# Kernel optimization log

Hardware: AMD Instinct MI355X
Metric: run time of the kernel (lower is better)

Reference implementation:

```python
import jax, jax.numpy as jnp
import numpy as np

N_NODES = 100000
N_EDGES = 1600000
D_IN = 128
D_HID = 128
D_OUT = 16


def gcn_conv(x, W, b, src, dst, deg_inv_sqrt, deg_inv):
    # PyG GCNConv: transform then normalized aggregate with self-loops.
    h = x @ W  # [N, H]
    norm = deg_inv_sqrt[src] * deg_inv_sqrt[dst]  # [E]
    msg = h[src] * norm[:, None]  # [E, H] gather
    agg = jax.ops.segment_sum(msg, dst, num_segments=N_NODES)  # scatter-add
    agg = agg + h * deg_inv[:, None]  # self-loop term (weight deg^-1)
    return agg + b


def setup_inputs() -> dict:
    key = jax.random.key(0)
    ks = jax.random.split(key, 10)
    x = jax.random.normal(ks[0], (N_NODES, D_IN), dtype=jnp.float32)
    edge_index = jax.random.randint(ks[1], (2, N_EDGES), 0, N_NODES)
    s = 1.0 / np.sqrt(D_IN)
    sh = 1.0 / np.sqrt(D_HID)
    W0 = jax.random.uniform(ks[2], (D_IN, D_HID), jnp.float32, -s, s)
    b0 = jnp.zeros((D_HID,), jnp.float32)
    W1 = jax.random.uniform(ks[3], (D_HID, D_HID), jnp.float32, -sh, sh)
    b1 = jnp.zeros((D_HID,), jnp.float32)
    W2 = jax.random.uniform(ks[4], (D_HID, D_HID), jnp.float32, -sh, sh)
    b2 = jnp.zeros((D_HID,), jnp.float32)
    Wr = jax.random.uniform(ks[5], (D_HID, D_OUT), jnp.float32, -sh, sh)
    br = jax.random.uniform(ks[6], (D_OUT,), jnp.float32, -sh, sh)
    return {"x": x, "edge_index": edge_index, "W0": W0, "b0": b0,
            "W1": W1, "b1": b1, "W2": W2, "b2": b2, "Wr": Wr, "br": br}


def reference(x, edge_index, W0, b0, W1, b1, W2, b2, Wr, br):
    src, dst = edge_index[0], edge_index[1]
    # degree with self-loops: deg[i] = 1 + indegree(i)
    deg = jax.ops.segment_sum(jnp.ones((N_EDGES,), x.dtype), dst,
                              num_segments=N_NODES) + 1.0
    deg_inv_sqrt = deg ** -0.5
    deg_inv = 1.0 / deg
    h = x
    for W, b in ((W0, b0), (W1, b1), (W2, b2)):
        h = gcn_conv(h, W, b, src, dst, deg_inv_sqrt, deg_inv)
        h = jax.nn.relu(h)  # dropout is identity at inference
    out = h @ Wr + br
    return jax.nn.sigmoid(out) * 0.8 + 0.1
```

## Files before the change

kernel.cpp:

```cpp
#include <hip/hip_runtime.h>
#include <math.h>

#define N_NODES 100000
#define N_EDGES 1600000
#define NBUCKET 782
#define EB      256
#define EPB     6250


static __device__ __forceinline__ unsigned short f2bf(float f) {
    unsigned int u = __float_as_uint(f);
    unsigned int r = (u + 0x7FFFu + ((u >> 16) & 1u)) >> 16;
    return (unsigned short)r;
}
static __device__ __forceinline__ float bf2f(unsigned short h) {
    return __uint_as_float(((unsigned int)h) << 16);
}


__global__ __launch_bounds__(256) void hist_kernel(const int* __restrict__ dst,
                                                   int* __restrict__ hist ) {
    __shared__ int h[NBUCKET];
    int tid = threadIdx.x;
    for (int b = tid; b < NBUCKET; b += 256) h[b] = 0;
    __syncthreads();
    int base = blockIdx.x * EPB;
    for (int i = tid; i < EPB; i += 256)
        atomicAdd(&h[dst[base + i] >> 7], 1);
    __syncthreads();
    int* hrow = hist + (size_t)blockIdx.x * NBUCKET;
    for (int b = tid; b < NBUCKET; b += 256) hrow[b] = h[b];
}

__global__ __launch_bounds__(256) void scan_hist_kernel(const int* __restrict__ hist,
                                                        int* __restrict__ blkoffT,
                                                        int* __restrict__ btotal) {
    __shared__ int s[256];
    int b = blockIdx.x;
    int k = threadIdx.x;
    int v = hist[(size_t)k * NBUCKET + b];
    s[k] = v;
    __syncthreads();
    for (int off = 1; off < 256; off <<= 1) {
        int t = 0;
        if (k >= off) t = s[k - off];
        __syncthreads();
        s[k] += t;
        __syncthreads();
    }
    blkoffT[(size_t)b * 256 + k] = s[k] - v;
    if (k == 255) btotal[b] = s[255];
}

__global__ __launch_bounds__(256) void bucket_scan_kernel(const int* __restrict__ btotal,
                                                          int* __restrict__ bucket_start) {
    __shared__ int cs[256];
    int tid = threadIdx.x;
    int base = tid * 4;
    int v[4];
    int sum = 0;
#pragma unroll
    for (int q = 0; q < 4; q++) {
        int idx = base + q;
        v[q] = (idx < NBUCKET) ? btotal[idx] : 0;
        sum += v[q];
    }
    cs[tid] = sum;
    __syncthreads();
    for (int off = 1; off < 256; off <<= 1) {
        int t = 0;
        if (tid >= off) t = cs[tid - off];
        __syncthreads();
        cs[tid] += t;
        __syncthreads();
    }
    int run = cs[tid] - sum;
#pragma unroll
    for (int q = 0; q < 4; q++) {
        int idx = base + q;
        if (idx < NBUCKET + 1) bucket_start[idx] = run;
        run += v[q];
    }
}

__global__ __launch_bounds__(256) void scatter_kernel(const int* __restrict__ src,
                                                      const int* __restrict__ dst,
                                                      const int* __restrict__ blkoffT,
                                                      const int* __restrict__ bucket_start,
                                                      int* __restrict__ pairs) {
    __shared__ int cur[NBUCKET];
    int tid = threadIdx.x;
    for (int b = tid; b < NBUCKET; b += 256)
        cur[b] = bucket_start[b] + blkoffT[(size_t)b * 256 + blockIdx.x];
    __syncthreads();
    int base = blockIdx.x * EPB;
    for (int i = tid; i < EPB; i += 256) {
        int d = dst[base + i];
        int s = src[base + i];
        int pos = atomicAdd(&cur[d >> 7], 1);
        pairs[pos] = s | ((d & 127) << 20);
    }
}

__global__ __launch_bounds__(256) void build_csr_kernel(const int* __restrict__ pairs,
                                                        const int* __restrict__ bucket_start,
                                                        int* __restrict__ rowstart,
                                                        int* __restrict__ counts,
                                                        float* __restrict__ dis,
                                                        int* __restrict__ csr_src) {
    __shared__ int lcnt[128];
    __shared__ int lsc[128];
    __shared__ int lcur[128];
    int tid = threadIdx.x;
    int b = blockIdx.x;
    int node_base = b * 128;
    if (tid < 128) lcnt[tid] = 0;
    __syncthreads();
    int rs = bucket_start[b];
    int re = bucket_start[b + 1];
    for (int e = rs + tid; e < re; e += 256)
        atomicAdd(&lcnt[pairs[e] >> 20], 1);
    __syncthreads();
    if (tid < 128) lsc[tid] = lcnt[tid];
    __syncthreads();
    for (int off = 1; off < 128; off <<= 1) {
        int t = 0;
        if (tid < 128 && tid >= off) t = lsc[tid - off];
        __syncthreads();
        if (tid < 128) lsc[tid] += t;
        __syncthreads();
    }
    if (tid < 128) {
        int node = node_base + tid;
        if (node < N_NODES) {
            int startg = rs + lsc[tid] - lcnt[tid];
            rowstart[node] = startg;
            counts[node]   = lcnt[tid];
            dis[node]      = rsqrtf((float)(lcnt[tid] + 1));
            lcur[tid]      = startg;
        }
    }
    __syncthreads();
    for (int e = rs + tid; e < re; e += 256) {
        int v = pairs[e];
        int pos = atomicAdd(&lcur[v >> 20], 1);
        csr_src[pos] = v & 0xFFFFF;
    }
}


__global__ __launch_bounds__(256) void gemm128_kernel(const float* __restrict__ X,
                                                      const float* __restrict__ W,
                                                      const float* __restrict__ scale,
                                                      unsigned short* __restrict__ Yb,
                                                      int nrows) {
    __shared__ float As[16][132];
    __shared__ float Bs[16][128];
    int tid = threadIdx.x;
    int tx = tid & 15;
    int ty = tid >> 4;
    int rowBase = blockIdx.x * 128;

    float acc[8][8];
#pragma unroll
    for (int i = 0; i < 8; i++)
#pragma unroll
        for (int j = 0; j < 8; j++) acc[i][j] = 0.f;

    int a_r  = tid >> 1;
    int a_k4 = (tid & 1) * 8;

    for (int kb = 0; kb < 128; kb += 16) {
        {
            int grow = rowBase + a_r;
            float4 v0 = make_float4(0.f,0.f,0.f,0.f), v1 = v0;
            if (grow < nrows) {
                v0 = *(const float4*)&X[(size_t)grow * 128 + kb + a_k4];
                v1 = *(const float4*)&X[(size_t)grow * 128 + kb + a_k4 + 4];
            }
            As[a_k4 + 0][a_r] = v0.x; As[a_k4 + 1][a_r] = v0.y;
            As[a_k4 + 2][a_r] = v0.z; As[a_k4 + 3][a_r] = v0.w;
            As[a_k4 + 4][a_r] = v1.x; As[a_k4 + 5][a_r] = v1.y;
            As[a_k4 + 6][a_r] = v1.z; As[a_k4 + 7][a_r] = v1.w;
        }
        {
            int f0 = tid, f1 = tid + 256;
            *(float4*)&Bs[f0 >> 5][(f0 & 31) * 4] =
                *(const float4*)&W[(size_t)(kb + (f0 >> 5)) * 128 + (f0 & 31) * 4];
            *(float4*)&Bs[f1 >> 5][(f1 & 31) * 4] =
                *(const float4*)&W[(size_t)(kb + (f1 >> 5)) * 128 + (f1 & 31) * 4];
        }
        __syncthreads();
#pragma unroll
        for (int kk = 0; kk < 16; kk++) {
            float4 a0 = *(const float4*)&As[kk][ty * 8];
            float4 a1 = *(const float4*)&As[kk][ty * 8 + 4];
            float4 b0 = *(const float4*)&Bs[kk][tx * 8];
            float4 b1 = *(const float4*)&Bs[kk][tx * 8 + 4];
            float a[8] = {a0.x,a0.y,a0.z,a0.w,a1.x,a1.y,a1.z,a1.w};
            float b[8] = {b0.x,b0.y,b0.z,b0.w,b1.x,b1.y,b1.z,b1.w};
#pragma unroll
            for (int i = 0; i < 8; i++)
#pragma unroll
                for (int j = 0; j < 8; j++) acc[i][j] = fmaf(a[i], b[j], acc[i][j]);
        }
        __syncthreads();
    }
#pragma unroll
    for (int i = 0; i < 8; i++) {
        int grow = rowBase + ty * 8 + i;
        if (grow < nrows) {
            float s = scale[grow];
            unsigned int p0 = (unsigned int)f2bf(acc[i][0]*s) | ((unsigned int)f2bf(acc[i][1]*s) << 16);
            unsigned int p1 = (unsigned int)f2bf(acc[i][2]*s) | ((unsigned int)f2bf(acc[i][3]*s) << 16);
            unsigned int p2 = (unsigned int)f2bf(acc[i][4]*s) | ((unsigned int)f2bf(acc[i][5]*s) << 16);
            unsigned int p3 = (unsigned int)f2bf(acc[i][6]*s) | ((unsigned int)f2bf(acc[i][7]*s) << 16);
            uint4 pk = make_uint4(p0, p1, p2, p3);
            *(uint4*)&Yb[(size_t)grow * 128 + tx * 8] = pk;
        }
    }
}


__global__ __launch_bounds__(256) void aggregate_kernel(const unsigned short* __restrict__ Hs,
                                                        const float* __restrict__ dis,
                                                        const int* __restrict__ rowstart,
                                                        const int* __restrict__ counts,
                                                        const int* __restrict__ csr_src,
                                                        const float* __restrict__ bias,
                                                        float* __restrict__ Out) {
    int node = blockIdx.x * 4 + (threadIdx.x >> 6);
    node = __builtin_amdgcn_readfirstlane(node);
    int lane = threadIdx.x & 63;
    if (node >= N_NODES) return;
    int c0 = lane * 2;

    unsigned int ow = *(const unsigned int*)&Hs[(size_t)node * 128 + c0];
    float accx = bf2f((unsigned short)(ow & 0xffffu));
    float accy = bf2f((unsigned short)(ow >> 16));

    int start = rowstart[node];
    int cnt   = counts[node];
    int end = start + cnt;
    int j = start;

    for (; j + 7 < end; j += 8) {
        int s0 = __builtin_nontemporal_load(&csr_src[j]);
        int s1 = __builtin_nontemporal_load(&csr_src[j + 1]);
        int s2 = __builtin_nontemporal_load(&csr_src[j + 2]);
        int s3 = __builtin_nontemporal_load(&csr_src[j + 3]);
        int s4 = __builtin_nontemporal_load(&csr_src[j + 4]);
        int s5 = __builtin_nontemporal_load(&csr_src[j + 5]);
        int s6 = __builtin_nontemporal_load(&csr_src[j + 6]);
        int s7 = __builtin_nontemporal_load(&csr_src[j + 7]);
        unsigned int w0 = *(const unsigned int*)&Hs[(size_t)s0 * 128 + c0];
        unsigned int w1 = *(const unsigned int*)&Hs[(size_t)s1 * 128 + c0];
        unsigned int w2 = *(const unsigned int*)&Hs[(size_t)s2 * 128 + c0];
        unsigned int w3 = *(const unsigned int*)&Hs[(size_t)s3 * 128 + c0];
        unsigned int w4 = *(const unsigned int*)&Hs[(size_t)s4 * 128 + c0];
        unsigned int w5 = *(const unsigned int*)&Hs[(size_t)s5 * 128 + c0];
        unsigned int w6 = *(const unsigned int*)&Hs[(size_t)s6 * 128 + c0];
        unsigned int w7 = *(const unsigned int*)&Hs[(size_t)s7 * 128 + c0];
        accx += ((bf2f((unsigned short)(w0 & 0xffffu)) + bf2f((unsigned short)(w1 & 0xffffu)))
               + (bf2f((unsigned short)(w2 & 0xffffu)) + bf2f((unsigned short)(w3 & 0xffffu))))
              + ((bf2f((unsigned short)(w4 & 0xffffu)) + bf2f((unsigned short)(w5 & 0xffffu)))
               + (bf2f((unsigned short)(w6 & 0xffffu)) + bf2f((unsigned short)(w7 & 0xffffu))));
        accy += ((bf2f((unsigned short)(w0 >> 16)) + bf2f((unsigned short)(w1 >> 16)))
               + (bf2f((unsigned short)(w2 >> 16)) + bf2f((unsigned short)(w3 >> 16))))
              + ((bf2f((unsigned short)(w4 >> 16)) + bf2f((unsigned short)(w5 >> 16)))
               + (bf2f((unsigned short)(w6 >> 16)) + bf2f((unsigned short)(w7 >> 16))));
    }
    for (; j + 1 < end; j += 2) {
        int s0 = __builtin_nontemporal_load(&csr_src[j]);
        int s1 = __builtin_nontemporal_load(&csr_src[j + 1]);
        unsigned int w0 = *(const unsigned int*)&Hs[(size_t)s0 * 128 + c0];
        unsigned int w1 = *(const unsigned int*)&Hs[(size_t)s1 * 128 + c0];
        accx += bf2f((unsigned short)(w0 & 0xffffu)) + bf2f((unsigned short)(w1 & 0xffffu));
        accy += bf2f((unsigned short)(w0 >> 16)) + bf2f((unsigned short)(w1 >> 16));
    }
    if (j < end) {
        int s0 = __builtin_nontemporal_load(&csr_src[j]);
        unsigned int w0 = *(const unsigned int*)&Hs[(size_t)s0 * 128 + c0];
        accx += bf2f((unsigned short)(w0 & 0xffffu));
        accy += bf2f((unsigned short)(w0 >> 16));
    }

    float dsi = dis[node];
    float2 bb = *(const float2*)&bias[c0];
    float2 r;
    r.x = fmaxf(fmaf(accx, dsi, bb.x), 0.f);
    r.y = fmaxf(fmaf(accy, dsi, bb.y), 0.f);
    unsigned long long bits;
    __builtin_memcpy(&bits, &r, 8);
    __builtin_nontemporal_store(bits, (unsigned long long*)&Out[(size_t)node * 128 + c0]);
}


__global__ __launch_bounds__(256) void final_kernel(const float* __restrict__ H,
                                                    const float* __restrict__ Wr,
                                                    const float* __restrict__ br,
                                                    float* __restrict__ out) {
    __shared__ float hs[16][132];
    __shared__ float ws[128][16];
    int tid = threadIdx.x;
    int rowBase = blockIdx.x * 16;
    {
        int k  = tid & 127;
        int r0 = tid >> 7;
#pragma unroll
        for (int rr = 0; rr < 8; rr++) {
            int r = r0 + rr * 2;
            int grow = rowBase + r;
            hs[r][k] = (grow < N_NODES) ? H[(size_t)grow * 128 + k] : 0.f;
        }
#pragma unroll
        for (int q = 0; q < 8; q++) {
            int idx = q * 256 + tid;
            ws[idx >> 4][idx & 15] = Wr[idx];
        }
    }
    __syncthreads();
    int row = tid >> 4;
    int c   = tid & 15;
    float acc = br[c];
#pragma unroll
    for (int k = 0; k < 128; k++)
        acc = fmaf(hs[row][k], ws[k][c], acc);
    int grow = rowBase + row;
    if (grow < N_NODES) {
        float sg = 1.f / (1.f + expf(-acc));
        out[(size_t)grow * 16 + c] = 0.8f * sg + 0.1f;
    }
}


extern "C" void kernel_launch(void* const* d_in, const int* in_sizes, int n_in,
                              void* d_out, int out_size, void* d_ws, size_t ws_size,
                              hipStream_t stream) {
    const float* x  = (const float*)d_in[0];
    const int*   ei = (const int*)d_in[1];
    const int*   src = ei;
    const int*   dst = ei + N_EDGES;
    const float* W0 = (const float*)d_in[2];
    const float* b0 = (const float*)d_in[3];
    const float* W1 = (const float*)d_in[4];
    const float* b1 = (const float*)d_in[5];
    const float* W2 = (const float*)d_in[6];
    const float* b2 = (const float*)d_in[7];
    const float* Wr = (const float*)d_in[8];
    const float* br = (const float*)d_in[9];
    float* out = (float*)d_out;

    char* ws = (char*)d_ws;
    size_t off = 0;
    auto take = [&](size_t bytes) {
        char* p = ws + off;
        off += (bytes + 255) & ~(size_t)255;
        return p;
    };
    float*          hA       = (float*)take((size_t)N_NODES * 128 * 4);
    unsigned short* hBs      = (unsigned short*)take((size_t)N_NODES * 128 * 2);
    int*            counts   = (int*)take((size_t)N_NODES * 4);
    int*            rowstart = (int*)take((size_t)N_NODES * 4);
    float*          dis      = (float*)take((size_t)N_NODES * 4);
    int*            csr_src  = (int*)take((size_t)N_EDGES * 4);
    int*            pairs    = (int*)take((size_t)N_EDGES * 4);
    int*            hist     = (int*)take((size_t)EB * NBUCKET * 4);
    int*            blkoffT  = (int*)take((size_t)NBUCKET * EB * 4);
    int*            btotal   = (int*)take(1024 * 4);
    int*            bstart   = (int*)take(1024 * 4);
    (void)ws_size; (void)in_sizes; (void)n_in; (void)out_size;

    hist_kernel<<<EB, 256, 0, stream>>>(dst, hist);
    scan_hist_kernel<<<NBUCKET, 256, 0, stream>>>(hist, blkoffT, btotal);
    bucket_scan_kernel<<<1, 256, 0, stream>>>(btotal, bstart);
    scatter_kernel<<<EB, 256, 0, stream>>>(src, dst, blkoffT, bstart, pairs);
    build_csr_kernel<<<NBUCKET, 256, 0, stream>>>(pairs, bstart, rowstart, counts, dis, csr_src);

    const float* Wl[3] = {W0, W1, W2};
    const float* bl[3] = {b0, b1, b2};
    const float* hin = x;
    for (int l = 0; l < 3; l++) {
        gemm128_kernel<<<(N_NODES + 127) / 128, 256, 0, stream>>>(hin, Wl[l], dis, hBs, N_NODES);
        aggregate_kernel<<<N_NODES / 4, 256, 0, stream>>>(hBs, dis, rowstart, counts,
                                                          csr_src, bl[l], hA);
        hin = hA;
    }
    final_kernel<<<N_NODES / 16, 256, 0, stream>>>(hA, Wr, br, out);
}
```

Baseline: 543.7 us.

## Use bf16 MFMA GEMM and store hidden activations as bf16

Replaces the fp32 FMA tiled GEMM with a bf16 MFMA kernel (16x16x32) that uses swizzled LDS tiles. It adds conversion kernels for x and a transposed W. The aggregate kernel now writes bf16 activations instead of fp32, so the next GEMM and the final kernel read half the bytes. The cost is lower precision in the GEMM inputs and intermediate activations, plus extra conversion launches and scalar 2-byte stores in the GEMM epilogue.

```diff
diff --git a/kernel.cpp b/kernel.cpp
--- a/kernel.cpp
+++ b/kernel.cpp
@@ -7,6 +7,9 @@
 #define EB      256
 #define EPB     6250
 
+typedef __attribute__((ext_vector_type(8))) __bf16 bf16x8;
+typedef __attribute__((ext_vector_type(4))) float  f32x4;
+
 
 static __device__ __forceinline__ unsigned short f2bf(float f) {
     unsigned int u = __float_as_uint(f);
@@ -15,6 +18,22 @@
 }
 static __device__ __forceinline__ float bf2f(unsigned short h) {
     return __uint_as_float(((unsigned int)h) << 16);
+}
+
+
+__global__ __launch_bounds__(256) void xconv_kernel(const float* __restrict__ X,
+                                                    unsigned short* __restrict__ Xb) {
+    int i = (blockIdx.x * 256 + threadIdx.x) * 4;
+    float4 v = *(const float4*)&X[i];
+    unsigned int p0 = (unsigned int)f2bf(v.x) | ((unsigned int)f2bf(v.y) << 16);
+    unsigned int p1 = (unsigned int)f2bf(v.z) | ((unsigned int)f2bf(v.w) << 16);
+    *(uint2*)&Xb[i] = make_uint2(p0, p1);
+}
+
+__global__ void wconv_kernel(const float* __restrict__ W, unsigned short* __restrict__ Wt) {
+    int n = blockIdx.x;
+    int k = threadIdx.x;
+    Wt[n * 128 + k] = f2bf(W[k * 128 + n]);
 }
 
 
@@ -149,74 +168,81 @@
 }
 
 
-__global__ __launch_bounds__(256) void gemm128_kernel(const float* __restrict__ X,
-                                                      const float* __restrict__ W,
-                                                      const float* __restrict__ scale,
-                                                      unsigned short* __restrict__ Yb,
-                                                      int nrows) {
-    __shared__ float As[16][132];
-    __shared__ float Bs[16][128];
-    int tid = threadIdx.x;
-    int tx = tid & 15;
-    int ty = tid >> 4;
+__global__ __launch_bounds__(256) void gemm_mfma_kernel(const unsigned short* __restrict__ Xb,
+                                                        const unsigned short* __restrict__ Wt,
+                                                        const float* __restrict__ dis,
+                                                        unsigned short* __restrict__ Yb) {
+    __shared__ unsigned short Xs[128 * 128];
+    __shared__ unsigned short Ws[128 * 128];
+    int tid = threadIdx.x;
     int rowBase = blockIdx.x * 128;
 
-    float acc[8][8];
-#pragma unroll
-    for (int i = 0; i < 8; i++)
-#pragma unroll
-        for (int j = 0; j < 8; j++) acc[i][j] = 0.f;
-
-    int a_r  = tid >> 1;
-    int a_k4 = (tid & 1) * 8;
-
-    for (int kb = 0; kb < 128; kb += 16) {
-        {
-            int grow = rowBase + a_r;
-            float4 v0 = make_float4(0.f,0.f,0.f,0.f), v1 = v0;
-            if (grow < nrows) {
-                v0 = *(const float4*)&X[(size_t)grow * 128 + kb + a_k4];
-                v1 = *(const float4*)&X[(size_t)grow * 128 + kb + a_k4 + 4];
+    {
+        int srow = tid >> 1;
+        int sk0  = (tid & 1) * 64;
+        bool ok = (rowBase + srow) < N_NODES;
+        const unsigned short* xsrc = Xb + (size_t)(rowBase + srow) * 128 + sk0;
+        const unsigned short* wsrc = Wt + (size_t)srow * 128 + sk0;
+#pragma unroll
+        for (int i = 0; i < 8; i++) {
+            int k = sk0 + i * 8;
+            uint4 xv = ok ? *(const uint4*)(xsrc + i * 8) : make_uint4(0, 0, 0, 0);
+            uint4 wv = *(const uint4*)(wsrc + i * 8);
+            int eo = (srow * 128 + k) ^ ((srow & 7) << 3);
+            *(uint4*)&Xs[eo] = xv;
+            *(uint4*)&Ws[eo] = wv;
+        }
+    }
+    __syncthreads();
+
+    int lane = tid & 63;
+    int wv_  = tid >> 6;
+    int wrow = wv_ * 32;
+    int lr   = lane & 15;
+    int loct = lane >> 4;
+
+    f32x4 acc[2][8];
+#pragma unroll
+    for (int a = 0; a < 2; a++)
+#pragma unroll
+        for (int b = 0; b < 8; b++) acc[a][b] = (f32x4){0.f, 0.f, 0.f, 0.f};
+
+#pragma unroll
+    for (int s = 0; s < 4; s++) {
+        int kb = s * 32 + loct * 8;
+        bf16x8 afr[2];
+#pragma unroll
+        for (int t2 = 0; t2 < 2; t2++) {
+            int row = wrow + t2 * 16 + lr;
+            int eo = (row * 128 + kb) ^ ((row & 7) << 3);
+            afr[t2] = *(const bf16x8*)&Xs[eo];
+        }
+#pragma unroll
+        for (int tc = 0; tc < 8; tc++) {
+            int col = tc * 16 + lr;
+            int eo = (col * 128 + kb) ^ ((col & 7) << 3);
+            bf16x8 bfr = *(const bf16x8*)&Ws[eo];
+            acc[0][tc] = __builtin_amdgcn_mfma_f32_16x16x32_bf16(afr[0], bfr, acc[0][tc], 0, 0, 0);
+            acc[1][tc] = __builtin_amdgcn_mfma_f32_16x16x32_bf16(afr[1], bfr, acc[1][tc], 0, 0, 0);
+        }
+    }
+
+#pragma unroll
+    for (int t2 = 0; t2 < 2; t2++) {
+        int rbase = rowBase + wrow + t2 * 16 + (lane >> 4) * 4;
+        float sc[4];
+#pragma unroll
+        for (int r = 0; r < 4; r++)
+            sc[r] = (rbase + r < N_NODES) ? dis[rbase + r] : 0.f;
+#pragma unroll
+        for (int tc = 0; tc < 8; tc++) {
+            int col = tc * 16 + lr;
+#pragma unroll
+            for (int r = 0; r < 4; r++) {
+                int row = rbase + r;
+                if (row < N_NODES)
+                    Yb[(size_t)row * 128 + col] = f2bf(acc[t2][tc][r] * sc[r]);
             }
-            As[a_k4 + 0][a_r] = v0.x; As[a_k4 + 1][a_r] = v0.y;
-            As[a_k4 + 2][a_r] = v0.z; As[a_k4 + 3][a_r] = v0.w;
-            As[a_k4 + 4][a_r] = v1.x; As[a_k4 + 5][a_r] = v1.y;
-            As[a_k4 + 6][a_r] = v1.z; As[a_k4 + 7][a_r] = v1.w;
-        }
-        {
-            int f0 = tid, f1 = tid + 256;
-            *(float4*)&Bs[f0 >> 5][(f0 & 31) * 4] =
-                *(const float4*)&W[(size_t)(kb + (f0 >> 5)) * 128 + (f0 & 31) * 4];
-            *(float4*)&Bs[f1 >> 5][(f1 & 31) * 4] =
-                *(const float4*)&W[(size_t)(kb + (f1 >> 5)) * 128 + (f1 & 31) * 4];
-        }
-        __syncthreads();
-#pragma unroll
-        for (int kk = 0; kk < 16; kk++) {
-            float4 a0 = *(const float4*)&As[kk][ty * 8];
-            float4 a1 = *(const float4*)&As[kk][ty * 8 + 4];
-            float4 b0 = *(const float4*)&Bs[kk][tx * 8];
-            float4 b1 = *(const float4*)&Bs[kk][tx * 8 + 4];
-            float a[8] = {a0.x,a0.y,a0.z,a0.w,a1.x,a1.y,a1.z,a1.w};
-            float b[8] = {b0.x,b0.y,b0.z,b0.w,b1.x,b1.y,b1.z,b1.w};
-#pragma unroll
-            for (int i = 0; i < 8; i++)
-#pragma unroll
-                for (int j = 0; j < 8; j++) acc[i][j] = fmaf(a[i], b[j], acc[i][j]);
-        }
-        __syncthreads();
-    }
-#pragma unroll
-    for (int i = 0; i < 8; i++) {
-        int grow = rowBase + ty * 8 + i;
-        if (grow < nrows) {
-            float s = scale[grow];
-            unsigned int p0 = (unsigned int)f2bf(acc[i][0]*s) | ((unsigned int)f2bf(acc[i][1]*s) << 16);
-            unsigned int p1 = (unsigned int)f2bf(acc[i][2]*s) | ((unsigned int)f2bf(acc[i][3]*s) << 16);
-            unsigned int p2 = (unsigned int)f2bf(acc[i][4]*s) | ((unsigned int)f2bf(acc[i][5]*s) << 16);
-            unsigned int p3 = (unsigned int)f2bf(acc[i][6]*s) | ((unsigned int)f2bf(acc[i][7]*s) << 16);
-            uint4 pk = make_uint4(p0, p1, p2, p3);
-            *(uint4*)&Yb[(size_t)grow * 128 + tx * 8] = pk;
         }
     }
 }
@@ -228,7 +254,7 @@
                                                         const int* __restrict__ counts,
                                                         const int* __restrict__ csr_src,
                                                         const float* __restrict__ bias,
-                                                        float* __restrict__ Out) {
+                                                        unsigned int* __restrict__ OutU) {
     int node = blockIdx.x * 4 + (threadIdx.x >> 6);
     node = __builtin_amdgcn_readfirstlane(node);
     int lane = threadIdx.x & 63;
@@ -287,16 +313,14 @@
 
     float dsi = dis[node];
     float2 bb = *(const float2*)&bias[c0];
-    float2 r;
-    r.x = fmaxf(fmaf(accx, dsi, bb.x), 0.f);
-    r.y = fmaxf(fmaf(accy, dsi, bb.y), 0.f);
-    unsigned long long bits;
-    __builtin_memcpy(&bits, &r, 8);
-    __builtin_nontemporal_store(bits, (unsigned long long*)&Out[(size_t)node * 128 + c0]);
-}
-
-
-__global__ __launch_bounds__(256) void final_kernel(const float* __restrict__ H,
+    float rx = fmaxf(fmaf(accx, dsi, bb.x), 0.f);
+    float ry = fmaxf(fmaf(accy, dsi, bb.y), 0.f);
+    unsigned int pk = (unsigned int)f2bf(rx) | ((unsigned int)f2bf(ry) << 16);
+    __builtin_nontemporal_store(pk, &OutU[(size_t)node * 64 + lane]);
+}
+
+
+__global__ __launch_bounds__(256) void final_kernel(const unsigned short* __restrict__ Hb,
                                                     const float* __restrict__ Wr,
                                                     const float* __restrict__ br,
                                                     float* __restrict__ out) {
@@ -305,13 +329,14 @@
     int tid = threadIdx.x;
     int rowBase = blockIdx.x * 16;
     {
-        int k  = tid & 127;
-        int r0 = tid >> 7;
-#pragma unroll
-        for (int rr = 0; rr < 8; rr++) {
-            int r = r0 + rr * 2;
-            int grow = rowBase + r;
-            hs[r][k] = (grow < N_NODES) ? H[(size_t)grow * 128 + k] : 0.f;
+#pragma unroll
+        for (int q = 0; q < 4; q++) {
+            int idx = q * 256 + tid;
+            int r  = idx >> 6;
+            int kp = (idx & 63) * 2;
+            unsigned int w = *(const unsigned int*)&Hb[(size_t)(rowBase + r) * 128 + kp];
+            hs[r][kp]     = bf2f((unsigned short)(w & 0xffffu));
+            hs[r][kp + 1] = bf2f((unsigned short)(w >> 16));
         }
 #pragma unroll
         for (int q = 0; q < 8; q++) {
@@ -327,10 +352,8 @@
     for (int k = 0; k < 128; k++)
         acc = fmaf(hs[row][k], ws[k][c], acc);
     int grow = rowBase + row;
-    if (grow < N_NODES) {
-        float sg = 1.f / (1.f + expf(-acc));
-        out[(size_t)grow * 16 + c] = 0.8f * sg + 0.1f;
-    }
+    float sg = 1.f / (1.f + expf(-acc));
+    out[(size_t)grow * 16 + c] = 0.8f * sg + 0.1f;
 }
 
 
@@ -358,8 +381,10 @@
         off += (bytes + 255) & ~(size_t)255;
         return p;
     };
-    float*          hA       = (float*)take((size_t)N_NODES * 128 * 4);
+    unsigned short* hAb      = (unsigned short*)take((size_t)N_NODES * 128 * 2);
     unsigned short* hBs      = (unsigned short*)take((size_t)N_NODES * 128 * 2);
+    unsigned short* xb       = (unsigned short*)take((size_t)N_NODES * 128 * 2);
+    unsigned short* Wt       = (unsigned short*)take(128 * 128 * 2);
     int*            counts   = (int*)take((size_t)N_NODES * 4);
     int*            rowstart = (int*)take((size_t)N_NODES * 4);
     float*          dis      = (float*)take((size_t)N_NODES * 4);
@@ -371,6 +396,8 @@
     int*            bstart   = (int*)take(1024 * 4);
     (void)ws_size; (void)in_sizes; (void)n_in; (void)out_size;
 
+    xconv_kernel<<<12500, 256, 0, stream>>>(x, xb);
+
     hist_kernel<<<EB, 256, 0, stream>>>(dst, hist);
     scan_hist_kernel<<<NBUCKET, 256, 0, stream>>>(hist, blkoffT, btotal);
     bucket_scan_kernel<<<1, 256, 0, stream>>>(btotal, bstart);
@@ -379,12 +406,13 @@
 
     const float* Wl[3] = {W0, W1, W2};
     const float* bl[3] = {b0, b1, b2};
-    const float* hin = x;
+    const unsigned short* hin = xb;
     for (int l = 0; l < 3; l++) {
-        gemm128_kernel<<<(N_NODES + 127) / 128, 256, 0, stream>>>(hin, Wl[l], dis, hBs, N_NODES);
+        wconv_kernel<<<128, 128, 0, stream>>>(Wl[l], Wt);
+        gemm_mfma_kernel<<<(N_NODES + 127) / 128, 256, 0, stream>>>(hin, Wt, dis, hBs);
         aggregate_kernel<<<N_NODES / 4, 256, 0, stream>>>(hBs, dis, rowstart, counts,
-                                                          csr_src, bl[l], hA);
-        hin = hA;
-    }
-    final_kernel<<<N_NODES / 16, 256, 0, stream>>>(hA, Wr, br, out);
-}
+                                                          csr_src, bl[l], (unsigned int*)hAb);
+        hin = hAb;
+    }
+    final_kernel<<<N_NODES / 16, 256, 0, stream>>>(hAb, Wr, br, out);
+}
```

Result: faster. 478.5 us (-12.0%).
